# Performance work log

Hardware: AMD Instinct MI355X
Metric: run time of the kernel (lower is better)

## Reference

```python
import jax, jax.numpy as jnp
import numpy as np

N_CLAUSES = 200000
N_FEATURES = 64
HIDDEN = 128
N_STEPS = 512


def setup_inputs() -> dict:
    key = jax.random.key(0)
    ks = jax.random.split(key, 8)
    features = jax.random.normal(ks[0], (N_CLAUSES, N_FEATURES), jnp.float32)
    W1 = jax.random.normal(ks[1], (N_FEATURES, HIDDEN), jnp.float32) / np.sqrt(N_FEATURES)
    b1 = jnp.zeros((HIDDEN,), jnp.float32)
    W2 = jax.random.normal(ks[2], (HIDDEN, HIDDEN), jnp.float32) / np.sqrt(HIDDEN)
    b2 = jnp.zeros((HIDDEN,), jnp.float32)
    key_w = jax.random.normal(ks[3], (HIDDEN,), jnp.float32) / np.sqrt(HIDDEN)
    # sel_mask[s, n] = clause n is in the passive set at SEL step s
    sel_mask = jax.random.bernoulli(ks[4], 0.5, (N_STEPS, N_CLAUSES))
    # proof_mask[n] = clause n participates in the final proof (sparse)
    proof_mask = jax.random.bernoulli(ks[5], 0.02, (N_CLAUSES,))
    # guarantee passive & proof nonempty at every step (torch code divides by its size)
    proof_mask = proof_mask.at[0].set(True)
    sel_mask = sel_mask.at[:, 0].set(True)
    return {
        "features": features, "W1": W1, "b1": b1, "W2": W2, "b2": b2,
        "key_w": key_w, "sel_mask": sel_mask, "proof_mask": proof_mask,
    }


def reference(features, W1, b1, W2, b2, key_w, sel_mask, proof_mask):
    # clause_embedder: 2-layer MLP; clause_key: dot with key vector -> one logit per clause
    h = jax.nn.relu(features @ W1 + b1)          # [N, H]
    emb = h @ W2 + b2                            # [N, H]
    logits = emb @ key_w                         # [N]

    neg = jnp.finfo(logits.dtype).min
    masked = jnp.where(sel_mask, logits[None, :], neg)   # [S, N]
    lse = jax.nn.logsumexp(masked, axis=1)                # [S] log-softmax denominator over passive set

    tgt = sel_mask & proof_mask[None, :]                  # [S, N] passive & proof
    cnt = tgt.sum(axis=1).astype(logits.dtype)            # [S] (>=1 by construction)
    # soft-target CE: -sum_j t_j * log_softmax(logits)_j, t uniform over tgt
    num = jnp.where(tgt, logits[None, :], 0.0).sum(axis=1) / cnt
    loss = (lse - num).mean()                             # mean over SEL steps
    return loss
```

## Files before the change

### kernel.cpp

```cpp
#include <hip/hip_runtime.h>
#include <hip/hip_bf16.h>

#define DEV __device__ __forceinline__

constexpr int NC = 200000;
constexpr int NF = 64;
constexpr int NH = 128;
constexpr int NS = 512;

constexpr int OF_CFG   = 0;
constexpr int OF_W1    = 16;
constexpr int OF_B1    = OF_W1 + NF * NH;
constexpr int OF_W2K   = OF_B1 + NH;
constexpr int OF_B2K   = OF_W2K + NH;
constexpr int OF_MAX   = OF_B2K + 1;
constexpr int OF_ACCE  = OF_MAX + 1;
constexpr int OF_ACCP  = OF_ACCE + NS;
constexpr int OF_ACCC  = OF_ACCP + NS;
constexpr int OF_LOGIT = 16384;
constexpr int OF_E     = OF_LOGIT + NC;
constexpr int OF_PL    = OF_E + NC;
constexpr int OF_PC    = OF_PL + NC;

DEV float bf2f(unsigned short u) { return __uint_as_float(((unsigned)u) << 16); }

DEV float loadF(const void* p, int i, int fk) {
    return fk ? bf2f(((const unsigned short*)p)[i]) : ((const float*)p)[i];
}

DEV unsigned flipf(float x) {
    unsigned u = __float_as_uint(x);
    return (u & 0x80000000u) ? ~u : (u | 0x80000000u);
}
DEV float unflipf(unsigned u) {
    unsigned b = (u & 0x80000000u) ? (u ^ 0x80000000u) : ~u;
    return __uint_as_float(b);
}

DEV bool okhalf(unsigned h) { return h == 0u || h == 1u || h == 0x3F80u || h == 0x3C00u; }

__global__ void k_probe(const void* features, const void* W1, const void* b1,
                        const void* W2, const void* b2, const void* keyw,
                        const void* sel, float* ws) {
    __shared__ int scfg[2];
    __shared__ float kw[NH];
    int tx = threadIdx.x;
    if (tx == 0) {
        const unsigned short* u = (const unsigned short*)features;
        int tiny = 0;
        for (int i = 0; i < 256; i++) {
            unsigned e = (u[i] >> 7) & 0xFFu;
            if (e < 100u) tiny++;
        }
        scfg[0] = (tiny >= 8) ? 0 : 1;
        const unsigned* w = (const unsigned*)sel;
        bool w4 = true, w2 = true;
        for (int i = 0; i < 256; i++) {
            unsigned v = w[i];
            if (!(v == 0u || v == 1u || v == 0x3F800000u)) w4 = false;
            if (!(okhalf(v & 0xFFFFu) && okhalf(v >> 16))) w2 = false;
        }
        scfg[1] = w4 ? 4 : (w2 ? 2 : 1);
    }
    __syncthreads();
    int fk = scfg[0];
    if (tx < 2) ((int*)ws)[tx] = scfg[tx];
    if (tx < NH) kw[tx] = loadF(keyw, tx, fk);
    for (int i = tx; i < NF * NH; i += blockDim.x) ws[OF_W1 + i] = loadF(W1, i, fk);
    if (tx < NH) ws[OF_B1 + tx] = loadF(b1, tx, fk);
    __syncthreads();
    if (tx < NH) {
        float s = 0.f;
        for (int k = 0; k < NH; k++) s += loadF(W2, tx * NH + k, fk) * kw[k];
        ws[OF_W2K + tx] = s;
    }
    if (tx == 0) {
        float s = 0.f;
        for (int k = 0; k < NH; k++) s += loadF(b2, k, fk) * kw[k];
        ws[OF_B2K] = s;
        ((unsigned*)ws)[OF_MAX] = 0u;
    }
    for (int i = tx; i < 3 * NS; i += blockDim.x) ws[OF_ACCE + i] = 0.f;
}

__global__ __launch_bounds__(256) void k_logits(const void* features, float* ws) {
    __shared__ float sW1[NF * NH];
    __shared__ float sB1[NH];
    __shared__ float sWK[NH];
    __shared__ float sred[4];
    int tx = threadIdx.x;
    int fk = ((const int*)ws)[0];
    for (int i = tx; i < NF * NH; i += 256) sW1[i] = ws[OF_W1 + i];
    if (tx < NH) { sB1[tx] = ws[OF_B1 + tx]; sWK[tx] = ws[OF_W2K + tx]; }
    float b2k = ws[OF_B2K];
    __syncthreads();
    int n = blockIdx.x * 256 + tx;
    float acc = -3.0e38f;
    if (n < NC) {
        float feat[NF];
        if (fk) {
            const uint4* fp = (const uint4*)((const unsigned short*)features + (size_t)n * NF);
            #pragma unroll
            for (int q = 0; q < 8; q++) {
                uint4 v = fp[q];
                unsigned vv[4] = {v.x, v.y, v.z, v.w};
                #pragma unroll
                for (int h = 0; h < 4; h++) {
                    feat[q * 8 + h * 2 + 0] = __uint_as_float(vv[h] << 16);
                    feat[q * 8 + h * 2 + 1] = __uint_as_float(vv[h] & 0xFFFF0000u);
                }
            }
        } else {
            const float4* fp = (const float4*)((const float*)features + (size_t)n * NF);
            #pragma unroll
            for (int q = 0; q < 16; q++) {
                float4 v = fp[q];
                feat[q * 4 + 0] = v.x; feat[q * 4 + 1] = v.y;
                feat[q * 4 + 2] = v.z; feat[q * 4 + 3] = v.w;
            }
        }
        acc = b2k;
        #pragma unroll 2
        for (int jc = 0; jc < NH / 4; jc++) {
            float d0 = sB1[jc * 4 + 0], d1 = sB1[jc * 4 + 1];
            float d2 = sB1[jc * 4 + 2], d3 = sB1[jc * 4 + 3];
            #pragma unroll
            for (int f = 0; f < NF; f++) {
                float4 w = *(const float4*)&sW1[f * NH + jc * 4];
                d0 += feat[f] * w.x; d1 += feat[f] * w.y;
                d2 += feat[f] * w.z; d3 += feat[f] * w.w;
            }
            acc += fmaxf(d0, 0.f) * sWK[jc * 4 + 0] + fmaxf(d1, 0.f) * sWK[jc * 4 + 1]
                 + fmaxf(d2, 0.f) * sWK[jc * 4 + 2] + fmaxf(d3, 0.f) * sWK[jc * 4 + 3];
        }
        ws[OF_LOGIT + n] = acc;
    }
    float m = acc;
    #pragma unroll
    for (int k = 1; k < 64; k <<= 1) m = fmaxf(m, __shfl_xor(m, k, 64));
    if ((tx & 63) == 0) sred[tx >> 6] = m;
    __syncthreads();
    if (tx == 0) {
        m = fmaxf(fmaxf(sred[0], sred[1]), fmaxf(sred[2], sred[3]));
        atomicMax((unsigned*)ws + OF_MAX, flipf(m));
    }
}

__global__ void k_prep(const void* proof, float* ws) {
    int n = blockIdx.x * 256 + threadIdx.x;
    if (n >= NC) return;
    int mw = ((const int*)ws)[1];
    float M = unflipf(((const unsigned*)ws)[OF_MAX]);
    float l = ws[OF_LOGIT + n];
    ws[OF_E + n] = __expf(l - M);
    bool pf;
    if (mw == 1)      pf = ((const unsigned char*)proof)[n] != 0;
    else if (mw == 2) pf = ((const unsigned short*)proof)[n] != 0;
    else              pf = ((const unsigned*)proof)[n] != 0;
    ws[OF_PL + n] = pf ? l : 0.f;
    ws[OF_PC + n] = pf ? 1.f : 0.f;
}

constexpr int NT_N = 16;
constexpr int BL_N = 256 * NT_N;
constexpr int SG = 32;

template<int MW>
DEV void bloop(const void* sel, int s0, int baddr,
               const float (&e)[NT_N], const float (&pl)[NT_N], const float (&pc)[NT_N],
               float* ws) {
    for (int si = 0; si < SG; si++) {
        int s = s0 + si;
        size_t off = (size_t)s * NC + (size_t)baddr;
        float m[NT_N];
        if (MW == 1) {
            uint4 w = *(const uint4*)((const unsigned char*)sel + off);
            unsigned v[4] = {w.x, w.y, w.z, w.w};
            #pragma unroll
            for (int q = 0; q < 4; q++)
                #pragma unroll
                for (int b = 0; b < 4; b++)
                    m[q * 4 + b] = ((v[q] >> (8 * b)) & 0xFFu) ? 1.f : 0.f;
        } else if (MW == 2) {
            const uint4* p = (const uint4*)((const unsigned short*)sel + off);
            #pragma unroll
            for (int h = 0; h < 2; h++) {
                uint4 w = p[h];
                unsigned v[4] = {w.x, w.y, w.z, w.w};
                #pragma unroll
                for (int q = 0; q < 4; q++) {
                    m[h * 8 + q * 2 + 0] = (v[q] & 0xFFFFu) ? 1.f : 0.f;
                    m[h * 8 + q * 2 + 1] = (v[q] >> 16) ? 1.f : 0.f;
                }
            }
        } else {
            const uint4* p = (const uint4*)((const unsigned*)sel + off);
            #pragma unroll
            for (int q = 0; q < 4; q++) {
                uint4 w = p[q];
                m[q * 4 + 0] = w.x ? 1.f : 0.f; m[q * 4 + 1] = w.y ? 1.f : 0.f;
                m[q * 4 + 2] = w.z ? 1.f : 0.f; m[q * 4 + 3] = w.w ? 1.f : 0.f;
            }
        }
        float se = 0.f, sp = 0.f, sc = 0.f;
        #pragma unroll
        for (int i = 0; i < NT_N; i++) {
            se += m[i] * e[i]; sp += m[i] * pl[i]; sc += m[i] * pc[i];
        }
        #pragma unroll
        for (int k = 1; k < 64; k <<= 1) {
            se += __shfl_xor(se, k, 64);
            sp += __shfl_xor(sp, k, 64);
            sc += __shfl_xor(sc, k, 64);
        }
        if ((threadIdx.x & 63) == 0) {
            atomicAdd(&ws[OF_ACCE + s], se);
            atomicAdd(&ws[OF_ACCP + s], sp);
            atomicAdd(&ws[OF_ACCC + s], sc);
        }
    }
}

__global__ __launch_bounds__(256) void k_phaseB(const void* sel, float* ws) {
    int tx = threadIdx.x;
    int base = blockIdx.x * BL_N + tx * NT_N;
    int s0 = blockIdx.y * SG;
    bool active = base < NC;
    int baddr = active ? base : 0;
    float e[NT_N], pl[NT_N], pc[NT_N];
    #pragma unroll
    for (int q = 0; q < 4; q++) {
        float4 ve = active ? ((const float4*)&ws[OF_E + baddr])[q]  : make_float4(0, 0, 0, 0);
        float4 vp = active ? ((const float4*)&ws[OF_PL + baddr])[q] : make_float4(0, 0, 0, 0);
        float4 vc = active ? ((const float4*)&ws[OF_PC + baddr])[q] : make_float4(0, 0, 0, 0);
        e[q * 4 + 0] = ve.x; e[q * 4 + 1] = ve.y; e[q * 4 + 2] = ve.z; e[q * 4 + 3] = ve.w;
        pl[q * 4 + 0] = vp.x; pl[q * 4 + 1] = vp.y; pl[q * 4 + 2] = vp.z; pl[q * 4 + 3] = vp.w;
        pc[q * 4 + 0] = vc.x; pc[q * 4 + 1] = vc.y; pc[q * 4 + 2] = vc.z; pc[q * 4 + 3] = vc.w;
    }
    int mw = ((const int*)ws)[1];
    if (mw == 1)      bloop<1>(sel, s0, baddr, e, pl, pc, ws);
    else if (mw == 2) bloop<2>(sel, s0, baddr, e, pl, pc, ws);
    else              bloop<4>(sel, s0, baddr, e, pl, pc, ws);
}

__global__ void k_final(float* ws, void* out) {
    __shared__ float sred[256];
    int tx = threadIdx.x;
    float M = unflipf(((const unsigned*)ws)[OF_MAX]);
    float sum = 0.f;
    for (int s = tx; s < NS; s += 256) {
        float lse = M + logf(ws[OF_ACCE + s]);
        sum += lse - ws[OF_ACCP + s] / ws[OF_ACCC + s];
    }
    sred[tx] = sum;
    __syncthreads();
    for (int k = 128; k > 0; k >>= 1) {
        if (tx < k) sred[tx] += sred[tx + k];
        __syncthreads();
    }
    if (tx == 0) {
        float loss = sred[0] / (float)NS;
        int fk = ((const int*)ws)[0];
        if (fk) ((__hip_bfloat16*)out)[0] = __float2bfloat16(loss);
        else    ((float*)out)[0] = loss;
    }
}

extern "C" void kernel_launch(void* const* d_in, const int* in_sizes, int n_in,
                              void* d_out, int out_size, void* d_ws, size_t ws_size,
                              hipStream_t stream) {
    const void* features = d_in[0];
    const void* W1   = d_in[1];
    const void* b1   = d_in[2];
    const void* W2   = d_in[3];
    const void* b2   = d_in[4];
    const void* keyw = d_in[5];
    const void* sel  = d_in[6];
    const void* proof = d_in[7];
    float* ws = (float*)d_ws;

    k_probe<<<1, 256, 0, stream>>>(features, W1, b1, W2, b2, keyw, sel, ws);
    int nblk = (NC + 255) / 256;
    k_logits<<<nblk, 256, 0, stream>>>(features, ws);
    k_prep<<<nblk, 256, 0, stream>>>(proof, ws);
    dim3 gB((NC + BL_N - 1) / BL_N, NS / SG);
    k_phaseB<<<gB, 256, 0, stream>>>(sel, ws);
    k_final<<<1, 256, 0, stream>>>(ws, d_out);
}
```

Before: 767.0 us.

## Read transposed W1 via uniform global loads and parallelize probe setup

k_probe now stores W1 transposed into jc-major float4 chunks, so k_logits can read weights straight from global memory with wave-uniform (scalar) loads. This drops the 32KB shared-memory staging and its barrier, which reduces LDS pressure and should raise occupancy. The probe's serial 256-iteration format detection and the b2·key dot product are now spread across threads using shared atomics and a small reduction. The cost is reliance on cache hits for the weight loads, and losing the shared staging may change scheduling.

```diff
diff --git a/kernel.cpp b/kernel.cpp
--- a/kernel.cpp
+++ b/kernel.cpp
@@ -42,58 +42,61 @@
 __global__ void k_probe(const void* features, const void* W1, const void* b1,
                         const void* W2, const void* b2, const void* keyw,
                         const void* sel, float* ws) {
-    __shared__ int scfg[2];
+    __shared__ int s_tiny, s_w4, s_w2;
     __shared__ float kw[NH];
-    int tx = threadIdx.x;
-    if (tx == 0) {
+    __shared__ float pr[NH];
+    int tx = threadIdx.x;
+    if (tx == 0) { s_tiny = 0; s_w4 = 1; s_w2 = 1; }
+    __syncthreads();
+    {
         const unsigned short* u = (const unsigned short*)features;
-        int tiny = 0;
-        for (int i = 0; i < 256; i++) {
-            unsigned e = (u[i] >> 7) & 0xFFu;
-            if (e < 100u) tiny++;
-        }
-        scfg[0] = (tiny >= 8) ? 0 : 1;
+        unsigned e = (u[tx] >> 7) & 0xFFu;
+        if (e < 100u) atomicAdd(&s_tiny, 1);
         const unsigned* w = (const unsigned*)sel;
-        bool w4 = true, w2 = true;
-        for (int i = 0; i < 256; i++) {
-            unsigned v = w[i];
-            if (!(v == 0u || v == 1u || v == 0x3F800000u)) w4 = false;
-            if (!(okhalf(v & 0xFFFFu) && okhalf(v >> 16))) w2 = false;
-        }
-        scfg[1] = w4 ? 4 : (w2 ? 2 : 1);
-    }
-    __syncthreads();
-    int fk = scfg[0];
-    if (tx < 2) ((int*)ws)[tx] = scfg[tx];
+        unsigned v = w[tx];
+        if (!(v == 0u || v == 1u || v == 0x3F800000u)) atomicAnd(&s_w4, 0);
+        if (!(okhalf(v & 0xFFFFu) && okhalf(v >> 16))) atomicAnd(&s_w2, 0);
+    }
+    __syncthreads();
+    int fk = (s_tiny >= 8) ? 0 : 1;
+    int mw = s_w4 ? 4 : (s_w2 ? 2 : 1);
+    if (tx == 0) { ((int*)ws)[0] = fk; ((int*)ws)[1] = mw; }
     if (tx < NH) kw[tx] = loadF(keyw, tx, fk);
-    for (int i = tx; i < NF * NH; i += blockDim.x) ws[OF_W1 + i] = loadF(W1, i, fk);
+    for (int i = tx; i < NF * NH; i += blockDim.x) {
+        int f = i >> 7;
+        int j = i & (NH - 1);
+        int jc = j >> 2, c = j & 3;
+        ws[OF_W1 + ((jc * NF + f) << 2) + c] = loadF(W1, i, fk);
+    }
     if (tx < NH) ws[OF_B1 + tx] = loadF(b1, tx, fk);
     __syncthreads();
     if (tx < NH) {
         float s = 0.f;
         for (int k = 0; k < NH; k++) s += loadF(W2, tx * NH + k, fk) * kw[k];
         ws[OF_W2K + tx] = s;
-    }
+        pr[tx] = loadF(b2, tx, fk) * kw[tx];
+    }
+    __syncthreads();
     if (tx == 0) {
         float s = 0.f;
-        for (int k = 0; k < NH; k++) s += loadF(b2, k, fk) * kw[k];
+        for (int k = 0; k < NH; k++) s += pr[k];
         ws[OF_B2K] = s;
         ((unsigned*)ws)[OF_MAX] = 0u;
     }
     for (int i = tx; i < 3 * NS; i += blockDim.x) ws[OF_ACCE + i] = 0.f;
 }
 
-__global__ __launch_bounds__(256) void k_logits(const void* features, float* ws) {
-    __shared__ float sW1[NF * NH];
-    __shared__ float sB1[NH];
-    __shared__ float sWK[NH];
+__global__ __launch_bounds__(256) void k_logits(const void* features,
+                                                const float* __restrict__ w1t,
+                                                const float* __restrict__ bias1,
+                                                const float* __restrict__ wk,
+                                                const float* __restrict__ cfg,
+                                                float* __restrict__ logits,
+                                                unsigned* __restrict__ maxp) {
     __shared__ float sred[4];
     int tx = threadIdx.x;
-    int fk = ((const int*)ws)[0];
-    for (int i = tx; i < NF * NH; i += 256) sW1[i] = ws[OF_W1 + i];
-    if (tx < NH) { sB1[tx] = ws[OF_B1 + tx]; sWK[tx] = ws[OF_W2K + tx]; }
-    float b2k = ws[OF_B2K];
-    __syncthreads();
+    int fk = ((const int*)cfg)[0];
+    float b2k = cfg[OF_B2K];
     int n = blockIdx.x * 256 + tx;
     float acc = -3.0e38f;
     if (n < NC) {
@@ -120,20 +123,21 @@
             }
         }
         acc = b2k;
-        #pragma unroll 2
         for (int jc = 0; jc < NH / 4; jc++) {
-            float d0 = sB1[jc * 4 + 0], d1 = sB1[jc * 4 + 1];
-            float d2 = sB1[jc * 4 + 2], d3 = sB1[jc * 4 + 3];
+            const float4* wp = (const float4*)(w1t + (size_t)jc * (NF * 4));
+            float4 b = *(const float4*)(bias1 + jc * 4);
+            float d0 = b.x, d1 = b.y, d2 = b.z, d3 = b.w;
             #pragma unroll
             for (int f = 0; f < NF; f++) {
-                float4 w = *(const float4*)&sW1[f * NH + jc * 4];
+                float4 w = wp[f];
                 d0 += feat[f] * w.x; d1 += feat[f] * w.y;
                 d2 += feat[f] * w.z; d3 += feat[f] * w.w;
             }
-            acc += fmaxf(d0, 0.f) * sWK[jc * 4 + 0] + fmaxf(d1, 0.f) * sWK[jc * 4 + 1]
-                 + fmaxf(d2, 0.f) * sWK[jc * 4 + 2] + fmaxf(d3, 0.f) * sWK[jc * 4 + 3];
-        }
-        ws[OF_LOGIT + n] = acc;
+            float4 k4 = *(const float4*)(wk + jc * 4);
+            acc += fmaxf(d0, 0.f) * k4.x + fmaxf(d1, 0.f) * k4.y
+                 + fmaxf(d2, 0.f) * k4.z + fmaxf(d3, 0.f) * k4.w;
+        }
+        logits[n] = acc;
     }
     float m = acc;
     #pragma unroll
@@ -142,7 +146,7 @@
     __syncthreads();
     if (tx == 0) {
         m = fmaxf(fmaxf(sred[0], sred[1]), fmaxf(sred[2], sred[3]));
-        atomicMax((unsigned*)ws + OF_MAX, flipf(m));
+        atomicMax(maxp, flipf(m));
     }
 }
 
@@ -281,7 +285,8 @@
 
     k_probe<<<1, 256, 0, stream>>>(features, W1, b1, W2, b2, keyw, sel, ws);
     int nblk = (NC + 255) / 256;
-    k_logits<<<nblk, 256, 0, stream>>>(features, ws);
+    k_logits<<<nblk, 256, 0, stream>>>(features, ws + OF_W1, ws + OF_B1, ws + OF_W2K,
+                                       ws, ws + OF_LOGIT, (unsigned*)ws + OF_MAX);
     k_prep<<<nblk, 256, 0, stream>>>(proof, ws);
     dim3 gB((NC + BL_N - 1) / BL_N, NS / SG);
     k_phaseB<<<gB, 256, 0, stream>>>(sel, ws);
```

Result: faster. 699.9 us (-8.8%).
